# Kernel tuning notes

Measured on AMD Instinct MI355X. Metric: run time of the kernel, lower is better.

The kernel has to match this reference:

```python
import jax, jax.numpy as jnp
import numpy as np

H = 16      # q heads
G = 4       # groups (n_rep)
THETA = 10000.0


def _rope(x, cos, sin):
    # x pairs adjacent elements (torch complex view of reshape(..., -1, 2))
    x0 = x[..., ::2]
    x1 = x[..., 1::2]
    r0 = x0 * cos - x1 * sin
    r1 = x0 * sin + x1 * cos
    return jnp.stack([r0, r1], axis=-1).reshape(x.shape)


def setup_inputs() -> dict:
    key = jax.random.key(0)
    ks = jax.random.split(key, 5)
    B, S, D = 2, 2048, 1024
    return {
        "x": jax.random.normal(ks[0], (B, S, D), jnp.float32),
        "Wq": jax.random.normal(ks[1], (D, D), jnp.float32) * 0.02,
        "Wk": jax.random.normal(ks[2], (D, D // G), jnp.float32) * 0.02,
        "Wv": jax.random.normal(ks[3], (D, D // G), jnp.float32) * 0.02,
        "Wo": jax.random.normal(ks[4], (D, D), jnp.float32) * 0.02,
    }


def reference(x, Wq, Wk, Wv, Wo):
    B, S, D = x.shape
    hd = D // H                     # head dim = 64
    Hkv = H // G                    # kv heads = 4

    q = x @ Wq                      # (B,S,D)
    k = x @ Wk                      # (B,S,D/G)
    v = x @ Wv                      # (B,S,D/G)

    # repeat_kv: (B,S,Hkv,hd) -> (B,S,H,hd)
    k = jnp.repeat(k.reshape(B, S, Hkv, hd), G, axis=2)
    v = jnp.repeat(v.reshape(B, S, Hkv, hd), G, axis=2)

    # RoPE angles: freqs precomputed over hidden_dim (as in source)
    inv = 1.0 / (THETA ** (jnp.arange(0, D, 2, dtype=jnp.float32) / D))  # (D/2,)
    ang = jnp.arange(S, dtype=jnp.float32)[:, None] * inv[None, :]       # (S,D/2)
    q = _rope(q, jnp.cos(ang)[None], jnp.sin(ang)[None])                 # (B,S,D)
    angk = ang[:, : hd // 2]                                             # (S,hd/2)
    k = _rope(k, jnp.cos(angk)[None, :, None, :], jnp.sin(angk)[None, :, None, :])

    q = q.reshape(B, S, H, hd).transpose(0, 2, 1, 3)   # (B,H,S,hd)
    k = k.transpose(0, 2, 1, 3)
    v = v.transpose(0, 2, 1, 3)

    # NOTE: scale uses sqrt(hidden_dim), faithful to source
    scores = jnp.einsum('bhqd,bhkd->bhqk', q, k) / jnp.sqrt(jnp.float32(D))
    p = jax.nn.softmax(scores, axis=-1)
    o = jnp.einsum('bhqk,bhkd->bhqd', p, v)
    o = o.transpose(0, 2, 1, 3).reshape(B, S, D)
    return o @ Wo
```

## Files before the change

### kernel.cpp

```cpp
#include <hip/hip_runtime.h>
#include <math.h>

#define BATCH 2
#define SEQ   2048
#define DMODEL 1024
#define KDIM  1024
#define NH    16
#define HDIM  64
#define GRP   4
#define NKV   4

enum { M_PLAIN = 0, M_QKV = 1 };

#define LN_THETA 9.210340371976184f

typedef short bf8_t __attribute__((ext_vector_type(8)));
typedef float f4_t __attribute__((ext_vector_type(4)));
typedef unsigned short us4_t __attribute__((ext_vector_type(4)));
typedef unsigned short us8_t __attribute__((ext_vector_type(8)));

#define QB_OFF 0
#define KB_OFF 4194304
#define VB_OFF (4194304 + 1048576)

__device__ __forceinline__ unsigned short f2bf(float f) {
  unsigned int u = __float_as_uint(f);
  u += 0x7fffu + ((u >> 16) & 1u);
  return (unsigned short)(u >> 16);
}

__device__ __forceinline__ void gload_lds16(const void* g, void* l) {
  typedef __attribute__((address_space(1))) unsigned int gu32;
  typedef __attribute__((address_space(3))) unsigned int lu32;
  __builtin_amdgcn_global_load_lds((const gu32*)g, (lu32*)l, 16, 0, 0);
}

__global__ __launch_bounds__(256) void conv_x(const float* __restrict__ in,
                                              unsigned short* __restrict__ out) {
  const int i = blockIdx.x * 256 + threadIdx.x;
  float4 v = ((const float4*)in)[i];
  us4_t o = {f2bf(v.x), f2bf(v.y), f2bf(v.z), f2bf(v.w)};
  ((us4_t*)out)[i] = o;
}

__global__ __launch_bounds__(256) void convT(const float* __restrict__ W,
                                             unsigned short* __restrict__ out,
                                             int N, int rowoff) {
  __shared__ unsigned short T[64][72];
  const int t = threadIdx.x;
  const int k0 = blockIdx.y * 64, n0 = blockIdx.x * 64;
  const int kr = t >> 4, n4 = (t & 15) * 4;
#pragma unroll
  for (int i = 0; i < 4; ++i) {
    const int k = kr + i * 16;
    float4 v = *(const float4*)&W[(size_t)(k0 + k) * N + n0 + n4];
    T[n4 + 0][k] = f2bf(v.x);
    T[n4 + 1][k] = f2bf(v.y);
    T[n4 + 2][k] = f2bf(v.z);
    T[n4 + 3][k] = f2bf(v.w);
  }
  __syncthreads();
#pragma unroll
  for (int i = 0; i < 2; ++i) {
    const int c = t + i * 256;
    const int n = c >> 3, kc = (c & 7) * 8;
    us8_t v = *(const us8_t*)&T[n][kc];
    *(us8_t*)&out[(size_t)(rowoff + n0 + n) * KDIM + k0 + kc] = v;
  }
}

template <int MODE>
__global__ __launch_bounds__(256, 3) void gemm_bf16(const unsigned short* __restrict__ A,
                                                    const unsigned short* __restrict__ Bt,
                                                    void* __restrict__ Cdst_, int N) {
  __shared__ __align__(16) unsigned short As[64 * 64];
  __shared__ __align__(16) unsigned short Bs[128 * 64];

  const int tid = threadIdx.x;
  const int lane = tid & 63, quad = lane >> 4, l16 = lane & 15;
  const int w = tid >> 6, wm = w >> 1, wn = w & 1;
  const int row0 = blockIdx.x * 64, col0 = blockIdx.y * 128;

  const int m0 = tid >> 2;
  const int kc0 = (tid & 3) ^ ((m0 >> 1) & 3);
  const unsigned short* Ag0 = A + (size_t)(row0 + m0) * KDIM + kc0 * 8;
  const unsigned short* Bg0 = Bt + (size_t)(col0 + m0) * KDIM + kc0 * 8;
  unsigned short* Al0 = &As[tid * 8];
  unsigned short* Bl0 = &Bs[tid * 8];

  int aoff[2][2], boff[4][2];
#pragma unroll
  for (int mi = 0; mi < 2; ++mi) {
    const int am = wm * 32 + mi * 16 + l16;
    const int sw = quad ^ ((am >> 1) & 3);
#pragma unroll
    for (int kh = 0; kh < 2; ++kh)
      aoff[mi][kh] = kh * 2048 + (((am << 2) | sw) << 3);
  }
#pragma unroll
  for (int ni = 0; ni < 4; ++ni) {
    const int bn = wn * 64 + ni * 16 + l16;
    const int sw = quad ^ ((bn >> 1) & 3);
#pragma unroll
    for (int kh = 0; kh < 2; ++kh)
      boff[ni][kh] = kh * 4096 + (((bn << 2) | sw) << 3);
  }

  f4_t acc[2][4];
#pragma unroll
  for (int mi = 0; mi < 2; ++mi)
#pragma unroll
    for (int ni = 0; ni < 4; ++ni) acc[mi][ni] = (f4_t){0.f, 0.f, 0.f, 0.f};

  for (int kb = 0; kb < KDIM; kb += 64) {
    __syncthreads();
    gload_lds16(Ag0 + kb,       Al0);
    gload_lds16(Ag0 + kb + 32,  Al0 + 2048);
    gload_lds16(Bg0 + kb,                     Bl0);
    gload_lds16(Bg0 + (size_t)64 * KDIM + kb, Bl0 + 2048);
    gload_lds16(Bg0 + kb + 32,                     Bl0 + 4096);
    gload_lds16(Bg0 + (size_t)64 * KDIM + kb + 32, Bl0 + 6144);
    __syncthreads();

    bf8_t af[2][2], bfr[4][2];
#pragma unroll
    for (int mi = 0; mi < 2; ++mi)
#pragma unroll
      for (int kh = 0; kh < 2; ++kh) af[mi][kh] = *(const bf8_t*)&As[aoff[mi][kh]];
#pragma unroll
    for (int ni = 0; ni < 4; ++ni)
#pragma unroll
      for (int kh = 0; kh < 2; ++kh) bfr[ni][kh] = *(const bf8_t*)&Bs[boff[ni][kh]];
#pragma unroll
    for (int kh = 0; kh < 2; ++kh)
#pragma unroll
      for (int mi = 0; mi < 2; ++mi)
#pragma unroll
        for (int ni = 0; ni < 4; ++ni)
          acc[mi][ni] = __builtin_amdgcn_mfma_f32_16x16x32_bf16(af[mi][kh], bfr[ni][kh], acc[mi][ni], 0, 0, 0);
  }

  if constexpr (MODE == M_PLAIN) {
    float* out = (float*)Cdst_;
#pragma unroll
    for (int mi = 0; mi < 2; ++mi) {
      const int rowb = row0 + wm * 32 + mi * 16 + quad * 4;
#pragma unroll
      for (int ni = 0; ni < 4; ++ni) {
        const int n = col0 + wn * 64 + ni * 16 + l16;
#pragma unroll
        for (int r = 0; r < 4; ++r)
          out[(size_t)(rowb + r) * N + n] = acc[mi][ni][r];
      }
    }
  } else {
    unsigned short* Qb = (unsigned short*)Cdst_;
    unsigned short* Kb = Qb + (KB_OFF - QB_OFF);
    unsigned short* Vb = Qb + (VB_OFF - QB_OFF);
#pragma unroll
    for (int ni = 0; ni < 4; ++ni) {
      const int nb = col0 + wn * 64 + ni * 16;
      const int n = nb + l16;
      if (nb < 1024) {
        const float inv = expf(-(float)(2 * (n >> 1)) * (LN_THETA / (float)DMODEL));
        const float sgn = (n & 1) ? 1.f : -1.f;
        const int h = n >> 6, d = n & 63;
#pragma unroll
        for (int mi = 0; mi < 2; ++mi) {
          const int rowb = row0 + wm * 32 + mi * 16 + quad * 4;
#pragma unroll
          for (int r = 0; r < 4; ++r) {
            const int row = rowb + r;
            const int bb = row >> 11, s = row & (SEQ - 1);
            const float v = acc[mi][ni][r];
            const float p = __shfl_xor(v, 1);
            float sn, cs;
            sincosf((float)s * inv, &sn, &cs);
            const float res = (v * cs + sgn * p * sn) * 0.03125f;
            Qb[((size_t)(bb * NH + h) * SEQ + s) * HDIM + d] = f2bf(res);
          }
        }
      } else if (nb < 1280) {
        const int nk = n - 1024;
        const int hkv = nk >> 6, d = nk & 63;
        const float inv = expf(-(float)(2 * (d >> 1)) * (LN_THETA / (float)DMODEL));
        const float sgn = (nk & 1) ? 1.f : -1.f;
#pragma unroll
        for (int mi = 0; mi < 2; ++mi) {
          const int rowb = row0 + wm * 32 + mi * 16 + quad * 4;
#pragma unroll
          for (int r = 0; r < 4; ++r) {
            const int row = rowb + r;
            const int bb = row >> 11, s = row & (SEQ - 1);
            const float v = acc[mi][ni][r];
            const float p = __shfl_xor(v, 1);
            float sn, cs;
            sincosf((float)s * inv, &sn, &cs);
            const float res = v * cs + sgn * p * sn;
            Kb[((size_t)(bb * NKV + hkv) * SEQ + s) * HDIM + d] = f2bf(res);
          }
        }
      } else {
        const int nv = n - 1280;
        const int hkv = nv >> 6, d = nv & 63;
#pragma unroll
        for (int mi = 0; mi < 2; ++mi) {
          const int s0 = row0 + wm * 32 + mi * 16 + quad * 4;
          const int bb = s0 >> 11, s = s0 & (SEQ - 1);
          us4_t st = {f2bf(acc[mi][ni][0]), f2bf(acc[mi][ni][1]),
                      f2bf(acc[mi][ni][2]), f2bf(acc[mi][ni][3])};
          *(us4_t*)&Vb[((size_t)(bb * NKV + hkv) * HDIM + d) * SEQ + s] = st;
        }
      }
    }
  }
}

__global__ __launch_bounds__(256, 4) void attn_fwd(const unsigned short* __restrict__ Q,
                                                   const unsigned short* __restrict__ K,
                                                   const unsigned short* __restrict__ V,
                                                   unsigned short* __restrict__ O) {
  __shared__ __align__(16) unsigned short Kt[64][72];
  __shared__ __align__(16) unsigned short Vt[64][72];
  __shared__ __align__(16) unsigned short Pt[4][16][72];

  const int b = blockIdx.y >> 4;
  const int h = blockIdx.y & (NH - 1);
  const int hkv = h >> 2;
  const int q0 = blockIdx.x * 64;
  const int tid = threadIdx.x;
  const int w = tid >> 6;
  const int lane = tid & 63;
  const int quad = lane >> 4;
  const int l16 = lane & 15;

  const unsigned short* Qg = Q + ((size_t)(b * NH + h) * SEQ + q0 + w * 16) * HDIM;
  const unsigned short* Kg = K + (size_t)(b * NKV + hkv) * SEQ * HDIM;
  const unsigned short* Vg = V + (size_t)(b * NKV + hkv) * HDIM * SEQ;

  const bf8_t qa0 = *(const bf8_t*)(Qg + (size_t)l16 * HDIM + quad * 8);
  const bf8_t qa1 = *(const bf8_t*)(Qg + (size_t)l16 * HDIM + 32 + quad * 8);

  bf8_t ones;
#pragma unroll
  for (int i = 0; i < 8; ++i) ones[i] = (short)0x3F80;

  f4_t accO[4];
#pragma unroll
  for (int d = 0; d < 4; ++d) accO[d] = (f4_t){0.f, 0.f, 0.f, 0.f};
  f4_t accL = (f4_t){0.f, 0.f, 0.f, 0.f};

  const int key = tid >> 2;
  const int dc = (tid & 3) * 8;

  for (int k0 = 0; k0 < SEQ; k0 += 64) {
    __syncthreads();
    *(bf8_t*)&Kt[key][dc]      = *(const bf8_t*)(Kg + (size_t)(k0 + key) * HDIM + dc);
    *(bf8_t*)&Kt[key][dc + 32] = *(const bf8_t*)(Kg + (size_t)(k0 + key) * HDIM + dc + 32);
    *(bf8_t*)&Vt[key][dc]      = *(const bf8_t*)(Vg + (size_t)key * SEQ + k0 + dc);
    *(bf8_t*)&Vt[key][dc + 32] = *(const bf8_t*)(Vg + (size_t)key * SEQ + k0 + dc + 32);
    __syncthreads();

#pragma unroll
    for (int cb = 0; cb < 4; ++cb) {
      bf8_t kf0 = *(const bf8_t*)&Kt[cb * 16 + l16][quad * 8];
      bf8_t kf1 = *(const bf8_t*)&Kt[cb * 16 + l16][32 + quad * 8];
      f4_t s = (f4_t){0.f, 0.f, 0.f, 0.f};
      s = __builtin_amdgcn_mfma_f32_16x16x32_bf16(qa0, kf0, s, 0, 0, 0);
      s = __builtin_amdgcn_mfma_f32_16x16x32_bf16(qa1, kf1, s, 0, 0, 0);
#pragma unroll
      for (int r = 0; r < 4; ++r)
        Pt[w][quad * 4 + r][cb * 16 + l16] = f2bf(__expf(s[r]));
    }

    bf8_t pa0 = *(const bf8_t*)&Pt[w][l16][quad * 8];
    bf8_t pa1 = *(const bf8_t*)&Pt[w][l16][32 + quad * 8];

    accL = __builtin_amdgcn_mfma_f32_16x16x32_bf16(pa0, ones, accL, 0, 0, 0);
    accL = __builtin_amdgcn_mfma_f32_16x16x32_bf16(pa1, ones, accL, 0, 0, 0);

#pragma unroll
    for (int db = 0; db < 4; ++db) {
      bf8_t vf0 = *(const bf8_t*)&Vt[db * 16 + l16][quad * 8];
      bf8_t vf1 = *(const bf8_t*)&Vt[db * 16 + l16][32 + quad * 8];
      accO[db] = __builtin_amdgcn_mfma_f32_16x16x32_bf16(pa0, vf0, accO[db], 0, 0, 0);
      accO[db] = __builtin_amdgcn_mfma_f32_16x16x32_bf16(pa1, vf1, accO[db], 0, 0, 0);
    }
  }

  float linv[4];
#pragma unroll
  for (int r = 0; r < 4; ++r) linv[r] = 1.0f / accL[r];

#pragma unroll
  for (int r = 0; r < 4; ++r) {
    const int q = q0 + w * 16 + quad * 4 + r;
    unsigned short* op = O + (((size_t)b * SEQ + q) * NH + h) * HDIM;
#pragma unroll
    for (int db = 0; db < 4; ++db)
      op[db * 16 + l16] = f2bf(accO[db][r] * linv[r]);
  }
}

extern "C" void kernel_launch(void* const* d_in, const int* in_sizes, int n_in,
                              void* d_out, int out_size, void* d_ws, size_t ws_size,
                              hipStream_t stream) {
  (void)in_sizes; (void)n_in; (void)out_size; (void)ws_size;
  const float* x  = (const float*)d_in[0];
  const float* Wq = (const float*)d_in[1];
  const float* Wk = (const float*)d_in[2];
  const float* Wv = (const float*)d_in[3];
  const float* Wo = (const float*)d_in[4];
  float* out = (float*)d_out;

  unsigned short* Qb    = (unsigned short*)d_ws;
  unsigned short* Kb    = Qb + 4194304;
  unsigned short* Vb    = Kb + 1048576;
  unsigned short* xb    = Vb + 1048576;
  unsigned short* Owb   = xb + 4194304;
  unsigned short* Wqkvt = Owb + 4194304;
  unsigned short* Wot   = Wqkvt + 1572864;

  dim3 blk(256);
  conv_x<<<dim3(4096), blk, 0, stream>>>(x, xb);
  convT<<<dim3(16, 16), blk, 0, stream>>>(Wq, Wqkvt, DMODEL, 0);
  convT<<<dim3(4, 16), blk, 0, stream>>>(Wk, Wqkvt, DMODEL / GRP, 1024);
  convT<<<dim3(4, 16), blk, 0, stream>>>(Wv, Wqkvt, DMODEL / GRP, 1280);
  convT<<<dim3(16, 16), blk, 0, stream>>>(Wo, Wot, DMODEL, 0);

  gemm_bf16<M_QKV><<<dim3(64, 12), blk, 0, stream>>>(xb, Wqkvt, Qb, 1536);
  attn_fwd<<<dim3(SEQ / 64, BATCH * NH), blk, 0, stream>>>(Qb, Kb, Vb, Owb);
  gemm_bf16<M_PLAIN><<<dim3(64, 8), blk, 0, stream>>>(Owb, Wot, out, DMODEL);
}
```

Measured before the change: 199.7 us.

## Process 32 query rows per wave in attention and swizzle LDS tiles

The attention kernel now has each wave handle two 16-row query groups (128 queries per block), so every K/V fragment read from LDS feeds twice as many MFMAs. LDS tiles switch from padded rows to an XOR-swizzled layout to avoid bank conflicts, P is written as 4-element vectors, and the QK MFMA operands are swapped so results land transposed. The grid is reordered so heads vary fastest, which should improve L2 reuse of K/V across blocks. Launch bounds drop to 2 blocks per SM, trading occupancy for more registers and less LDS traffic per FLOP.

```diff
diff --git a/kernel.cpp b/kernel.cpp
--- a/kernel.cpp
+++ b/kernel.cpp
@@ -216,90 +216,116 @@
   }
 }
 
-__global__ __launch_bounds__(256, 4) void attn_fwd(const unsigned short* __restrict__ Q,
+__global__ __launch_bounds__(256, 2) void attn_fwd(const unsigned short* __restrict__ Q,
                                                    const unsigned short* __restrict__ K,
                                                    const unsigned short* __restrict__ V,
                                                    unsigned short* __restrict__ O) {
-  __shared__ __align__(16) unsigned short Kt[64][72];
-  __shared__ __align__(16) unsigned short Vt[64][72];
-  __shared__ __align__(16) unsigned short Pt[4][16][72];
-
-  const int b = blockIdx.y >> 4;
-  const int h = blockIdx.y & (NH - 1);
+  __shared__ __align__(16) unsigned short Kt[4096];
+  __shared__ __align__(16) unsigned short Vt[4096];
+  __shared__ __align__(16) unsigned short Pt[4][2048];
+
+  const int b = blockIdx.x >> 4;
+  const int h = blockIdx.x & (NH - 1);
   const int hkv = h >> 2;
-  const int q0 = blockIdx.x * 64;
+  const int q0 = blockIdx.y * 128;
   const int tid = threadIdx.x;
   const int w = tid >> 6;
   const int lane = tid & 63;
   const int quad = lane >> 4;
   const int l16 = lane & 15;
 
-  const unsigned short* Qg = Q + ((size_t)(b * NH + h) * SEQ + q0 + w * 16) * HDIM;
+  const unsigned short* Qg = Q + ((size_t)(b * NH + h) * SEQ + q0 + w * 32) * HDIM;
   const unsigned short* Kg = K + (size_t)(b * NKV + hkv) * SEQ * HDIM;
   const unsigned short* Vg = V + (size_t)(b * NKV + hkv) * HDIM * SEQ;
 
-  const bf8_t qa0 = *(const bf8_t*)(Qg + (size_t)l16 * HDIM + quad * 8);
-  const bf8_t qa1 = *(const bf8_t*)(Qg + (size_t)l16 * HDIM + 32 + quad * 8);
+  bf8_t qb[2][2];
+#pragma unroll
+  for (int g = 0; g < 2; ++g)
+#pragma unroll
+    for (int half = 0; half < 2; ++half)
+      qb[g][half] = *(const bf8_t*)(Qg + (size_t)(g * 16 + l16) * HDIM + half * 32 + quad * 8);
 
   bf8_t ones;
 #pragma unroll
   for (int i = 0; i < 8; ++i) ones[i] = (short)0x3F80;
 
-  f4_t accO[4];
-#pragma unroll
-  for (int d = 0; d < 4; ++d) accO[d] = (f4_t){0.f, 0.f, 0.f, 0.f};
-  f4_t accL = (f4_t){0.f, 0.f, 0.f, 0.f};
-
-  const int key = tid >> 2;
-  const int dc = (tid & 3) * 8;
+  f4_t accO[2][4];
+#pragma unroll
+  for (int g = 0; g < 2; ++g)
+#pragma unroll
+    for (int d = 0; d < 4; ++d) accO[g][d] = (f4_t){0.f, 0.f, 0.f, 0.f};
+  f4_t accL[2] = {(f4_t){0.f, 0.f, 0.f, 0.f}, (f4_t){0.f, 0.f, 0.f, 0.f}};
+
+  const int x7 = l16 & 7;
+  const int kc0 = (quad ^ x7) << 3;
+  const int kc1 = kc0 ^ 32;
+  unsigned short* Ptw = Pt[w];
+
+  const int srow = tid >> 3;
+  const int sch = tid & 7;
 
   for (int k0 = 0; k0 < SEQ; k0 += 64) {
     __syncthreads();
-    *(bf8_t*)&Kt[key][dc]      = *(const bf8_t*)(Kg + (size_t)(k0 + key) * HDIM + dc);
-    *(bf8_t*)&Kt[key][dc + 32] = *(const bf8_t*)(Kg + (size_t)(k0 + key) * HDIM + dc + 32);
-    *(bf8_t*)&Vt[key][dc]      = *(const bf8_t*)(Vg + (size_t)key * SEQ + k0 + dc);
-    *(bf8_t*)&Vt[key][dc + 32] = *(const bf8_t*)(Vg + (size_t)key * SEQ + k0 + dc + 32);
+#pragma unroll
+    for (int i = 0; i < 2; ++i) {
+      const int row = srow + i * 32;
+      const int pcol = ((sch ^ (row & 7)) << 3);
+      *(bf8_t*)&Kt[row * 64 + pcol] = *(const bf8_t*)(Kg + (size_t)(k0 + row) * HDIM + sch * 8);
+      *(bf8_t*)&Vt[row * 64 + pcol] = *(const bf8_t*)(Vg + (size_t)row * SEQ + k0 + sch * 8);
+    }
     __syncthreads();
 
 #pragma unroll
     for (int cb = 0; cb < 4; ++cb) {
-      bf8_t kf0 = *(const bf8_t*)&Kt[cb * 16 + l16][quad * 8];
-      bf8_t kf1 = *(const bf8_t*)&Kt[cb * 16 + l16][32 + quad * 8];
-      f4_t s = (f4_t){0.f, 0.f, 0.f, 0.f};
-      s = __builtin_amdgcn_mfma_f32_16x16x32_bf16(qa0, kf0, s, 0, 0, 0);
-      s = __builtin_amdgcn_mfma_f32_16x16x32_bf16(qa1, kf1, s, 0, 0, 0);
-#pragma unroll
-      for (int r = 0; r < 4; ++r)
-        Pt[w][quad * 4 + r][cb * 16 + l16] = f2bf(__expf(s[r]));
-    }
-
-    bf8_t pa0 = *(const bf8_t*)&Pt[w][l16][quad * 8];
-    bf8_t pa1 = *(const bf8_t*)&Pt[w][l16][32 + quad * 8];
-
-    accL = __builtin_amdgcn_mfma_f32_16x16x32_bf16(pa0, ones, accL, 0, 0, 0);
-    accL = __builtin_amdgcn_mfma_f32_16x16x32_bf16(pa1, ones, accL, 0, 0, 0);
+      const int krow = (cb * 16 + l16) * 64;
+      bf8_t kf0 = *(const bf8_t*)&Kt[krow + kc0];
+      bf8_t kf1 = *(const bf8_t*)&Kt[krow + kc1];
+      const int pcol = (((cb * 2 + (quad >> 1)) ^ x7) << 3) + ((quad & 1) << 2);
+#pragma unroll
+      for (int g = 0; g < 2; ++g) {
+        f4_t s = (f4_t){0.f, 0.f, 0.f, 0.f};
+        s = __builtin_amdgcn_mfma_f32_16x16x32_bf16(kf0, qb[g][0], s, 0, 0, 0);
+        s = __builtin_amdgcn_mfma_f32_16x16x32_bf16(kf1, qb[g][1], s, 0, 0, 0);
+        us4_t p = {f2bf(__expf(s[0])), f2bf(__expf(s[1])),
+                   f2bf(__expf(s[2])), f2bf(__expf(s[3]))};
+        *(us4_t*)&Ptw[(g * 16 + l16) * 64 + pcol] = p;
+      }
+    }
+
+    bf8_t pa[2][2];
+#pragma unroll
+    for (int g = 0; g < 2; ++g) {
+      const int prow = (g * 16 + l16) * 64;
+      pa[g][0] = *(const bf8_t*)&Ptw[prow + kc0];
+      pa[g][1] = *(const bf8_t*)&Ptw[prow + kc1];
+      accL[g] = __builtin_amdgcn_mfma_f32_16x16x32_bf16(pa[g][0], ones, accL[g], 0, 0, 0);
+      accL[g] = __builtin_amdgcn_mfma_f32_16x16x32_bf16(pa[g][1], ones, accL[g], 0, 0, 0);
+    }
 
 #pragma unroll
     for (int db = 0; db < 4; ++db) {
-      bf8_t vf0 = *(const bf8_t*)&Vt[db * 16 + l16][quad * 8];
-      bf8_t vf1 = *(const bf8_t*)&Vt[db * 16 + l16][32 + quad * 8];
-      accO[db] = __builtin_amdgcn_mfma_f32_16x16x32_bf16(pa0, vf0, accO[db], 0, 0, 0);
-      accO[db] = __builtin_amdgcn_mfma_f32_16x16x32_bf16(pa1, vf1, accO[db], 0, 0, 0);
-    }
-  }
-
-  float linv[4];
-#pragma unroll
-  for (int r = 0; r < 4; ++r) linv[r] = 1.0f / accL[r];
-
-#pragma unroll
-  for (int r = 0; r < 4; ++r) {
-    const int q = q0 + w * 16 + quad * 4 + r;
-    unsigned short* op = O + (((size_t)b * SEQ + q) * NH + h) * HDIM;
-#pragma unroll
-    for (int db = 0; db < 4; ++db)
-      op[db * 16 + l16] = f2bf(accO[db][r] * linv[r]);
-  }
+      const int vrow = (db * 16 + l16) * 64;
+      bf8_t vf0 = *(const bf8_t*)&Vt[vrow + kc0];
+      bf8_t vf1 = *(const bf8_t*)&Vt[vrow + kc1];
+#pragma unroll
+      for (int g = 0; g < 2; ++g) {
+        accO[g][db] = __builtin_amdgcn_mfma_f32_16x16x32_bf16(pa[g][0], vf0, accO[g][db], 0, 0, 0);
+        accO[g][db] = __builtin_amdgcn_mfma_f32_16x16x32_bf16(pa[g][1], vf1, accO[g][db], 0, 0, 0);
+      }
+    }
+  }
+
+#pragma unroll
+  for (int g = 0; g < 2; ++g)
+#pragma unroll
+    for (int r = 0; r < 4; ++r) {
+      const float linv = 1.0f / accL[g][r];
+      const int q = q0 + w * 32 + g * 16 + quad * 4 + r;
+      unsigned short* op = O + (((size_t)b * SEQ + q) * NH + h) * HDIM;
+#pragma unroll
+      for (int db = 0; db < 4; ++db)
+        op[db * 16 + l16] = f2bf(accO[g][db][r] * linv);
+    }
 }
 
 extern "C" void kernel_launch(void* const* d_in, const int* in_sizes, int n_in,
@@ -329,6 +355,6 @@
   convT<<<dim3(16, 16), blk, 0, stream>>>(Wo, Wot, DMODEL, 0);
 
   gemm_bf16<M_QKV><<<dim3(64, 12), blk, 0, stream>>>(xb, Wqkvt, Qb, 1536);
-  attn_fwd<<<dim3(SEQ / 64, BATCH * NH), blk, 0, stream>>>(Qb, Kb, Vb, Owb);
+  attn_fwd<<<dim3(BATCH * NH, SEQ / 128), blk, 0, stream>>>(Qb, Kb, Vb, Owb);
   gemm_bf16<M_PLAIN><<<dim3(64, 8), blk, 0, stream>>>(Owb, Wot, out, DMODEL);
 }
```

New measurement: 199.7 us. Within noise of the previous version (-0.0%).
